# Optimization experiments

Hardware: AMD Instinct MI355X
Metric: run time of the kernel (lower is better)

The kernel has to match this reference:

```python
import jax, jax.numpy as jnp
import numpy as np

N, E, G, D = 50000, 500000, 100, 64
H = D // 64          # num_heads = emb_dim // 64 = 1
HD = D // H          # head_dim


def setup_inputs() -> dict:
    key = jax.random.key(0)
    ks = jax.random.split(key, 14)
    s = 0.05
    return {
        "x": jax.random.normal(ks[0], (N, D), jnp.float32),
        "edge_attr": jax.random.normal(ks[1], (E, D), jnp.float32),
        "u": jax.random.normal(ks[2], (G, D), jnp.float32),
        # params: torch Linear convention, weight is [out, in]
        "W_edge": jax.random.normal(ks[3], (D, 4 * D), jnp.float32) * s,
        "b_edge": jnp.zeros((D,), jnp.float32),
        "W_node": jax.random.normal(ks[4], (D, 4 * D), jnp.float32) * s,
        "b_node": jnp.zeros((D,), jnp.float32),
        "W_glob": jax.random.normal(ks[5], (D, 3 * D), jnp.float32) * s,
        "b_glob": jnp.zeros((D,), jnp.float32),
        # NodeAttn params: w1 Linear(3D->D), w2 [H, HD], w3 Linear(2D->D)
        "na_w1": jax.random.normal(ks[6], (D, 3 * D), jnp.float32) * s,
        "na_b1": jnp.zeros((D,), jnp.float32),
        "na_w2": jax.random.normal(ks[7], (H, HD), jnp.float32) * s,
        "na_w3": jax.random.normal(ks[8], (D, 2 * D), jnp.float32) * s,
        "na_b3": jnp.zeros((D,), jnp.float32),
        "edge_index": jax.random.randint(ks[9], (2, E), 0, N),
        "node_batch": jnp.sort(jax.random.randint(ks[10], (N,), 0, G)),
        "edge_batch": jnp.sort(jax.random.randint(ks[11], (E,), 0, G)),
    }


def reference(x, edge_attr, u, W_edge, b_edge, W_node, b_node, W_glob, b_glob,
              na_w1, na_b1, na_w2, na_w3, na_b3,
              edge_index, node_batch, edge_batch):
    row, col = edge_index[0], edge_index[1]

    # ---- edge model: gather + concat + MLP ----
    e_in = jnp.concatenate([edge_attr, x[row], x[col], u[edge_batch]], axis=1)  # [E, 4D]
    edge_new = jax.nn.relu(e_in @ W_edge.T + b_edge)                             # [E, D]

    # ---- NodeAttn: segment softmax attention, scatter-sum to nodes ----
    def node_attn(q, k_v, k_e, idx):
        h = (jnp.concatenate([q, k_v, k_e], axis=1) @ na_w1.T + na_b1)  # [E, D]
        h = jax.nn.leaky_relu(h.reshape(-1, H, HD))
        w = jnp.einsum('nhc,hc->nh', h, na_w2)[:, :, None]              # [E, H, 1]
        m = jax.ops.segment_max(w, idx, num_segments=N)
        ex = jnp.exp(w - m[idx])
        sm = jax.ops.segment_sum(ex, idx, num_segments=N)
        p = ex / (sm[idx] + 1e-16)                                      # segment softmax
        v = (jnp.concatenate([k_v, k_e], axis=1) @ na_w3.T + na_b3).reshape(-1, H, HD)
        return jax.ops.segment_sum((p * v).reshape(-1, D), idx, num_segments=N)

    sent = node_attn(x[row], x[col], edge_new, row)   # [N, D]
    recv = node_attn(x[col], x[row], edge_new, col)   # [N, D]

    # ---- node model ----
    n_in = jnp.concatenate([x, sent, recv, u[node_batch]], axis=1)  # [N, 4D]
    x_new = jax.nn.relu(n_in @ W_node.T + b_node)                   # [N, D]

    # ---- global model: scatter-aggregate nodes/edges per graph ----
    node_agg = jax.ops.segment_sum(x_new, node_batch, num_segments=G)
    edge_agg = jax.ops.segment_sum(edge_new, edge_batch, num_segments=G)
    g_in = jnp.concatenate([u, node_agg, edge_agg], axis=1)         # [G, 3D]
    u_new = jax.nn.relu(g_in @ W_glob.T + b_glob)                   # [G, D]

    return (x_new, edge_new, u_new)
```

## Files before the change

### kernel.cpp

```cpp
#include <hip/hip_runtime.h>

typedef __attribute__((ext_vector_type(8))) short bf16x8;
typedef __attribute__((ext_vector_type(4))) float f32x4;

#define MFMA16(A, B, C) __builtin_amdgcn_mfma_f32_16x16x32_bf16(A, B, C, 0, 0, 0)

__device__ __forceinline__ float4 ld4(const float* p) {
  return *reinterpret_cast<const float4*>(p);
}

__device__ __forceinline__ unsigned short f2bf(float f) {
  unsigned u = __float_as_uint(f);
  unsigned r = u + 0x7FFFu + ((u >> 16) & 1u);
  return (unsigned short)(r >> 16);
}

__device__ __forceinline__ float bf2f(unsigned short b) {
  return __uint_as_float(((unsigned)b) << 16);
}
__device__ __forceinline__ float bflo(unsigned u) { return __uint_as_float(u << 16); }
__device__ __forceinline__ float bfhi(unsigned u) { return __uint_as_float(u & 0xFFFF0000u); }
__device__ __forceinline__ unsigned bfpack(float lo, float hi) {
  return (unsigned)f2bf(lo) | ((unsigned)f2bf(hi) << 16);
}

__device__ __forceinline__ bf16x8 cvt8(float4 a, float4 b) {
  bf16x8 v;
  v[0] = (short)f2bf(a.x); v[1] = (short)f2bf(a.y);
  v[2] = (short)f2bf(a.z); v[3] = (short)f2bf(a.w);
  v[4] = (short)f2bf(b.x); v[5] = (short)f2bf(b.y);
  v[6] = (short)f2bf(b.z); v[7] = (short)f2bf(b.w);
  return v;
}

__global__ void __launch_bounds__(256) k_fill(
    const int* __restrict__ row, const int* __restrict__ col,
    int* __restrict__ deg_s, int* __restrict__ deg_r,
    int* __restrict__ lst_s, int* __restrict__ lst_r, int E) {
  int e = blockIdx.x * 256 + threadIdx.x;
  if (e >= E) return;
  int r = row[e], c = col[e];
  int s0 = atomicAdd(deg_s + r, 1);
  if (s0 < 64) lst_s[(size_t)r * 64 + s0] = e;
  int s1 = atomicAdd(deg_r + c, 1);
  if (s1 < 64) lst_r[(size_t)c * 64 + s1] = e;
}

__global__ void __launch_bounds__(128) k_precomb(
    const float* __restrict__ Wn, const float* __restrict__ W3, const float* __restrict__ b3,
    const float* __restrict__ We, const float* __restrict__ u_,
    float* __restrict__ Ms, float* __restrict__ cs,
    float* __restrict__ Mr, float* __restrict__ cr,
    float* __restrict__ pu, float* __restrict__ pun, int G) {
  int t = threadIdx.x;
  if (blockIdx.x < 8) {
    int dir = t >> 6, o = t & 63;
    const float* wrow = Wn + (size_t)o * 256 + 64 + 64 * dir;
    float* M  = dir ? Mr : Ms;
    float* cv = dir ? cr : cs;
    if (blockIdx.x == 0) {
      float cb = 0.f;
      for (int k = 0; k < 64; ++k) cb = fmaf(wrow[k], b3[k], cb);
      cv[o] = cb;
    }
    int c0 = blockIdx.x * 16;
    for (int c = c0; c < c0 + 16; ++c) {
      float m = 0.f;
      for (int k = 0; k < 64; ++k) m = fmaf(wrow[k], W3[k * 128 + c], m);
      M[(size_t)o * 128 + c] = m;
    }
  } else {
    const float* W = (blockIdx.x == 8) ? We : Wn;
    float* dst = (blockIdx.x == 8) ? pu : pun;
    int o = t & 63;
    const float* wr = W + (size_t)o * 256 + 192;
    for (int g = t >> 6; g < G; g += 2) {
      float a = 0.f;
      const float* uv = u_ + (size_t)g * 64;
      for (int k = 0; k < 64; ++k) a = fmaf(wr[k], uv[k], a);
      dst[(size_t)g * 64 + o] = a;
    }
  }
}

__global__ void __launch_bounds__(256) k_pack(
    const float* __restrict__ We, const float* __restrict__ W1, const float* __restrict__ Wn,
    const float* __restrict__ Ms, const float* __restrict__ Mr,
    unsigned short* __restrict__ BpP, unsigned short* __restrict__ BpN) {
  int idx = blockIdx.x * 256 + threadIdx.x;
  if (idx < 2048) {
    int lane = idx & 63, nt = (idx >> 6) & 15, ks = idx >> 10;
    int l15 = lane & 15, lg = lane >> 4;
    int c = nt * 16 + l15, a = c >> 6, o = c & 63;
    bf16x8 v;
    #pragma unroll
    for (int j = 0; j < 8; ++j) {
      int k = ks * 32 + lg * 8 + j;
      float f = (a == 0) ? We[o * 256 + 64 + k]
              : (a == 1) ? We[o * 256 + 128 + k]
              : (a == 2) ? W1[o * 192 + k]
                         : W1[o * 192 + 64 + k];
      v[j] = (short)f2bf(f);
    }
    *(bf16x8*)(BpP + (size_t)idx * 8) = v;
  } else if (idx < 2048 + 2560) {
    int i2 = idx - 2048;
    int lane = i2 & 63, nt = (i2 >> 6) & 3, ks = i2 >> 8;
    int l15 = lane & 15, lg = lane >> 4;
    int col = nt * 16 + l15;
    bf16x8 v;
    #pragma unroll
    for (int j = 0; j < 8; ++j) {
      int k = ks * 32 + lg * 8 + j;
      float f = (k < 64) ? Wn[col * 256 + k]
              : (k < 192) ? Ms[col * 128 + (k - 64)]
                          : Mr[col * 128 + (k - 192)];
      v[j] = (short)f2bf(f);
    }
    *(bf16x8*)(BpN + (size_t)i2 * 8) = v;
  }
}

__global__ void __launch_bounds__(256) k_nodepre4(
    const float* __restrict__ x, const unsigned short* __restrict__ BpP,
    unsigned int* __restrict__ pxx, unsigned int* __restrict__ hqk,
    unsigned short* __restrict__ x_bf, int N) {
  __shared__ unsigned short lB[2048 * 8];
  const int tid = threadIdx.x;
  for (int i = tid; i < 2048; i += 256)
    *(uint4*)(lB + (size_t)i * 8) = *(const uint4*)(BpP + (size_t)i * 8);
  __syncthreads();
  const int lane = tid & 63, wid = tid >> 6, l15 = lane & 15, lg = lane >> 4;
  const int n0 = (blockIdx.x * 4 + wid) * 16;
  if (n0 >= N) return;
  int arow = n0 + l15; if (arow >= N) arow = N - 1;
  const float* src = x + (size_t)arow * 64 + lg * 8;
  bf16x8 A0 = cvt8(ld4(src), ld4(src + 4));
  bf16x8 A1 = cvt8(ld4(src + 32), ld4(src + 36));
  if (n0 + l15 < N) {
    *(bf16x8*)(x_bf + (size_t)(n0 + l15) * 64 + lg * 8) = A0;
    *(bf16x8*)(x_bf + (size_t)(n0 + l15) * 64 + 32 + lg * 8) = A1;
  }
  f32x4 acc[16];
  #pragma unroll
  for (int nt = 0; nt < 16; ++nt) {
    acc[nt] = (f32x4){0.f, 0.f, 0.f, 0.f};
    acc[nt] = MFMA16(A0, *(const bf16x8*)(lB + ((size_t)(0 * 16 + nt) * 64 + lane) * 8), acc[nt]);
    acc[nt] = MFMA16(A1, *(const bf16x8*)(lB + ((size_t)(1 * 16 + nt) * 64 + lane) * 8), acc[nt]);
  }
  #pragma unroll
  for (int q = 0; q < 4; ++q) {
    const int o = q * 16 + l15;
    #pragma unroll
    for (int j = 0; j < 4; ++j) {
      int n = n0 + lg * 4 + j;
      if (n < N) {
        pxx[(size_t)n * 64 + o] = bfpack(acc[q][j],     acc[4 + q][j]);
        hqk[(size_t)n * 64 + o] = bfpack(acc[8 + q][j], acc[12 + q][j]);
      }
    }
  }
}

__global__ void __launch_bounds__(256, 2) k_edgeattn4(
    const float* __restrict__ ea,
    const unsigned int* __restrict__ pxx, const unsigned int* __restrict__ hqk,
    const float* __restrict__ pu,
    const float* __restrict__ We, const float* __restrict__ be,
    const float* __restrict__ W1, const float* __restrict__ b1, const float* __restrict__ w2,
    const int* __restrict__ row, const int* __restrict__ col, const int* __restrict__ ebat,
    float* __restrict__ edge_out, unsigned short* __restrict__ en_bf,
    float* __restrict__ w_s, float* __restrict__ w_r, int E) {
  __shared__ unsigned short enl_all[4][16 * 64];
  const int tid = threadIdx.x, lane = tid & 63, wid = tid >> 6;
  const int l15 = lane & 15, lg = lane >> 4;

  bf16x8 B1[4][2], B2[4][2];
  #pragma unroll
  for (int nt = 0; nt < 4; ++nt) {
    #pragma unroll
    for (int ks = 0; ks < 2; ++ks) {
      const float* s1 = We + (size_t)(nt * 16 + l15) * 256 + ks * 32 + lg * 8;
      B1[nt][ks] = cvt8(ld4(s1), ld4(s1 + 4));
      const float* s2 = W1 + (size_t)(nt * 16 + l15) * 192 + 128 + ks * 32 + lg * 8;
      B2[nt][ks] = cvt8(ld4(s2), ld4(s2 + 4));
    }
  }
  float be_l[4], b1_l[4], w2_l[4];
  #pragma unroll
  for (int nt = 0; nt < 4; ++nt) {
    be_l[nt] = be[nt * 16 + l15];
    b1_l[nt] = b1[nt * 16 + l15];
    w2_l[nt] = w2[nt * 16 + l15];
  }
  unsigned short* enl = enl_all[wid];
  const int nwaves = gridDim.x * 4;
  const int swz_r = (l15 & 7) << 4;

  for (int e0 = (blockIdx.x * 4 + wid) * 16; e0 < E; e0 += nwaves * 16) {
    int rj[4], cj[4], gj[4];
    if (e0 + 16 <= E) {
      int4 r4 = *(const int4*)(row + e0 + lg * 4);
      int4 c4 = *(const int4*)(col + e0 + lg * 4);
      int4 g4 = *(const int4*)(ebat + e0 + lg * 4);
      rj[0]=r4.x; rj[1]=r4.y; rj[2]=r4.z; rj[3]=r4.w;
      cj[0]=c4.x; cj[1]=c4.y; cj[2]=c4.z; cj[3]=c4.w;
      gj[0]=g4.x; gj[1]=g4.y; gj[2]=g4.z; gj[3]=g4.w;
    } else {
      #pragma unroll
      for (int j = 0; j < 4; ++j) {
        int ee = e0 + lg * 4 + j; if (ee >= E) ee = E - 1;
        rj[j] = row[ee]; cj[j] = col[ee]; gj[j] = ebat[ee];
      }
    }

    unsigned hr_[4][4], hc_[4][4], pr_[4][4], pc_[4][4];
    float puv[4][4];
    #pragma unroll
    for (int j = 0; j < 4; ++j) {
      #pragma unroll
      for (int nt = 0; nt < 4; ++nt) {
        const int o = nt * 16 + l15;
        hr_[j][nt] = hqk[(size_t)rj[j] * 64 + o];
        hc_[j][nt] = hqk[(size_t)cj[j] * 64 + o];
        pr_[j][nt] = pxx[(size_t)rj[j] * 64 + o];
        pc_[j][nt] = pxx[(size_t)cj[j] * 64 + o];
        puv[j][nt] = pu [(size_t)gj[j] * 64 + o];
      }
    }

    int erow = e0 + l15; if (erow >= E) erow = E - 1;
    const float* arow = ea + (size_t)erow * 64;
    bf16x8 A1[2];
    #pragma unroll
    for (int ks = 0; ks < 2; ++ks) {
      const float* s = arow + ks * 32 + lg * 8;
      A1[ks] = cvt8(ld4(s), ld4(s + 4));
    }

    f32x4 acc[4];
    #pragma unroll
    for (int nt = 0; nt < 4; ++nt) acc[nt] = (f32x4){0.f, 0.f, 0.f, 0.f};
    #pragma unroll
    for (int nt = 0; nt < 4; ++nt) {
      acc[nt] = MFMA16(A1[0], B1[nt][0], acc[nt]);
      acc[nt] = MFMA16(A1[1], B1[nt][1], acc[nt]);
    }

    #pragma unroll
    for (int j = 0; j < 4; ++j) {
      const int m = lg * 4 + j;
      const bool st = (e0 + m) < E;
      float* eo = edge_out + (size_t)(e0 + m) * 64 + l15;
      unsigned short* eb = en_bf + (size_t)(e0 + m) * 64 + l15;
      const int rbase = m * 128, sw = (m & 7) << 4;
      #pragma unroll
      for (int nt = 0; nt < 4; ++nt) {
        float v = acc[nt][j] + be_l[nt] + bflo(pr_[j][nt]) + bfhi(pc_[j][nt]) + puv[j][nt];
        v = fmaxf(v, 0.f);
        unsigned short bv = f2bf(v);
        if (st) { eo[nt * 16] = v; eb[nt * 16] = bv; }
        int byte = rbase + ((nt * 32 + l15 * 2) ^ sw);
        *(unsigned short*)((char*)enl + byte) = bv;
      }
    }

    asm volatile("s_waitcnt lgkmcnt(0)" ::: "memory");
    bf16x8 A2[2];
    #pragma unroll
    for (int ks = 0; ks < 2; ++ks) {
      int byte = l15 * 128 + (((ks * 64) + lg * 16) ^ swz_r);
      A2[ks] = *(const bf16x8*)((const char*)enl + byte);
    }

    f32x4 tac[4];
    #pragma unroll
    for (int nt = 0; nt < 4; ++nt) tac[nt] = (f32x4){0.f, 0.f, 0.f, 0.f};
    #pragma unroll
    for (int nt = 0; nt < 4; ++nt) {
      tac[nt] = MFMA16(A2[0], B2[nt][0], tac[nt]);
      tac[nt] = MFMA16(A2[1], B2[nt][1], tac[nt]);
    }

    float as4[4] = {0.f, 0.f, 0.f, 0.f}, ar4[4] = {0.f, 0.f, 0.f, 0.f};
    #pragma unroll
    for (int j = 0; j < 4; ++j) {
      #pragma unroll
      for (int nt = 0; nt < 4; ++nt) {
        float tt = tac[nt][j] + b1_l[nt];
        float hs = tt + bflo(hr_[j][nt]) + bfhi(hc_[j][nt]); hs = (hs >= 0.f) ? hs : 0.01f * hs;
        float hr2 = tt + bflo(hc_[j][nt]) + bfhi(hr_[j][nt]); hr2 = (hr2 >= 0.f) ? hr2 : 0.01f * hr2;
        as4[j] = fmaf(hs, w2_l[nt], as4[j]);
        ar4[j] = fmaf(hr2, w2_l[nt], ar4[j]);
      }
    }
    #pragma unroll
    for (int j = 0; j < 4; ++j) {
      #pragma unroll
      for (int d = 1; d < 16; d <<= 1) {
        as4[j] += __shfl_xor(as4[j], d, 64);
        ar4[j] += __shfl_xor(ar4[j], d, 64);
      }
    }
    if (l15 == 0) {
      #pragma unroll
      for (int j = 0; j < 4; ++j) {
        int e = e0 + lg * 4 + j;
        if (e < E) { w_s[e] = as4[j]; w_r[e] = ar4[j]; }
      }
    }
  }
}

__global__ void __launch_bounds__(256) k_gatherw2(
    const unsigned short* __restrict__ x_bf, const unsigned short* __restrict__ en_bf,
    const float* __restrict__ w_s, const float* __restrict__ w_r,
    const int* __restrict__ lst_s, const int* __restrict__ lst_r,
    const int* __restrict__ deg_s, const int* __restrict__ deg_r,
    const int* __restrict__ row, const int* __restrict__ col,
    unsigned short* __restrict__ ss_s, unsigned short* __restrict__ ss_r,
    float* __restrict__ gam_s, float* __restrict__ gam_r, int N) {
  const int dir = blockIdx.y;
  const float* w = dir ? w_r : w_s;
  const int* lst = dir ? lst_r : lst_s;
  const int* deg_a = dir ? deg_r : deg_s;
  const int* other_idx = dir ? row : col;
  unsigned short* ss = dir ? ss_r : ss_s;
  float* gam = dir ? gam_r : gam_s;

  int wid = threadIdx.x >> 6, lane = threadIdx.x & 63;
  int n = blockIdx.x * 4 + wid;
  if (n >= N) return;
  int deg = deg_a[n];
  deg = deg < 64 ? deg : 64;
  unsigned short* ssd = ss + (size_t)n * 128;
  if (deg == 0) {
    ssd[lane] = 0; ssd[64 + lane] = 0;
    if (lane == 0) gam[n] = 0.f;
    return;
  }
  int e = 0, oe = 0;
  float wv = -1e30f;
  if (lane < deg) {
    e = lst[(size_t)n * 64 + lane];
    oe = other_idx[e];
    wv = w[e];
  }
  float m = wv;
  #pragma unroll
  for (int d = 32; d; d >>= 1) m = fmaxf(m, __shfl_xor(m, d, 64));
  float p = (lane < deg) ? __expf(wv - m) : 0.f;
  float S = p;
  #pragma unroll
  for (int d = 32; d; d >>= 1) S += __shfl_xor(S, d, 64);
  float sx4[4] = {0.f, 0.f, 0.f, 0.f};
  float se4[4] = {0.f, 0.f, 0.f, 0.f};
  int i = 0;
  for (; i + 8 <= deg; i += 8) {
    float pp[8]; int oo[8], ee[8];
    #pragma unroll
    for (int k = 0; k < 8; ++k) {
      pp[k] = __shfl(p, i + k, 64);
      oo[k] = __shfl(oe, i + k, 64);
      ee[k] = __shfl(e, i + k, 64);
    }
    float xv[8], ev[8];
    #pragma unroll
    for (int k = 0; k < 8; ++k) {
      xv[k] = bf2f(x_bf[(size_t)oo[k] * 64 + lane]);
      ev[k] = bf2f(en_bf[(size_t)ee[k] * 64 + lane]);
    }
    #pragma unroll
    for (int k = 0; k < 8; ++k) {
      sx4[k & 3] = fmaf(pp[k], xv[k], sx4[k & 3]);
      se4[k & 3] = fmaf(pp[k], ev[k], se4[k & 3]);
    }
  }
  for (; i + 4 <= deg; i += 4) {
    float pp[4]; int oo[4], ee[4];
    #pragma unroll
    for (int k = 0; k < 4; ++k) {
      pp[k] = __shfl(p, i + k, 64);
      oo[k] = __shfl(oe, i + k, 64);
      ee[k] = __shfl(e, i + k, 64);
    }
    #pragma unroll
    for (int k = 0; k < 4; ++k) {
      sx4[k] = fmaf(pp[k], bf2f(x_bf[(size_t)oo[k] * 64 + lane]), sx4[k]);
      se4[k] = fmaf(pp[k], bf2f(en_bf[(size_t)ee[k] * 64 + lane]), se4[k]);
    }
  }
  for (; i < deg; ++i) {
    float pi = __shfl(p, i, 64);
    int ei = __shfl(e, i, 64);
    int oi = __shfl(oe, i, 64);
    sx4[0] = fmaf(pi, bf2f(x_bf[(size_t)oi * 64 + lane]), sx4[0]);
    se4[0] = fmaf(pi, bf2f(en_bf[(size_t)ei * 64 + lane]), se4[0]);
  }
  float sx = (sx4[0] + sx4[1]) + (sx4[2] + sx4[3]);
  float se = (se4[0] + se4[1]) + (se4[2] + se4[3]);
  float inv = 1.f / (S + 1e-16f);
  ssd[lane] = f2bf(sx * inv);
  ssd[64 + lane] = f2bf(se * inv);
  if (lane == 0) gam[n] = S * inv;
}

__global__ void __launch_bounds__(256) k_node4(
    const unsigned short* __restrict__ x_bf,
    const unsigned short* __restrict__ ss_s, const unsigned short* __restrict__ ss_r,
    const float* __restrict__ gam_s, const float* __restrict__ gam_r,
    const unsigned short* __restrict__ BpN,
    const float* __restrict__ bn, const float* __restrict__ cs, const float* __restrict__ cr,
    const float* __restrict__ pun, const int* __restrict__ nbat,
    float* __restrict__ x_out, int N) {
  __shared__ unsigned short lB[2560 * 8];
  const int tid = threadIdx.x;
  for (int i = tid; i < 2560; i += 256)
    *(uint4*)(lB + (size_t)i * 8) = *(const uint4*)(BpN + (size_t)i * 8);
  __syncthreads();
  const int lane = tid & 63, wid = tid >> 6, l15 = lane & 15, lg = lane >> 4;
  const int n0 = (blockIdx.x * 4 + wid) * 16;
  if (n0 >= N) return;
  int arow = n0 + l15; if (arow >= N) arow = N - 1;

  f32x4 acc[4];
  #pragma unroll
  for (int nt = 0; nt < 4; ++nt) acc[nt] = (f32x4){0.f, 0.f, 0.f, 0.f};

  #pragma unroll
  for (int ks = 0; ks < 10; ++ks) {
    const unsigned short* s;
    if (ks < 2)      s = x_bf + (size_t)arow * 64  + ks * 32 + lg * 8;
    else if (ks < 6) s = ss_s + (size_t)arow * 128 + (ks - 2) * 32 + lg * 8;
    else             s = ss_r + (size_t)arow * 128 + (ks - 6) * 32 + lg * 8;
    bf16x8 A = *(const bf16x8*)s;
    #pragma unroll
    for (int nt = 0; nt < 4; ++nt)
      acc[nt] = MFMA16(A, *(const bf16x8*)(lB + ((size_t)(ks * 4 + nt) * 64 + lane) * 8), acc[nt]);
  }

  #pragma unroll
  for (int j = 0; j < 4; ++j) {
    int n = n0 + lg * 4 + j;
    int nn = n < N ? n : N - 1;
    int g = nbat[nn];
    float gs = gam_s[nn], gr = gam_r[nn];
    #pragma unroll
    for (int nt = 0; nt < 4; ++nt) {
      int o = nt * 16 + l15;
      float v = acc[nt][j] + bn[o] + pun[(size_t)g * 64 + o] + gs * cs[o] + gr * cr[o];
      v = fmaxf(v, 0.f);
      if (n < N) x_out[(size_t)n * 64 + o] = v;
    }
  }
}

__global__ void __launch_bounds__(256) k_segsum(
    const float* __restrict__ vals, const int* __restrict__ seg,
    float* __restrict__ out, int n) {
  int d = threadIdx.x & 63;
  int grp = threadIdx.x >> 6;
  long base = (long)blockIdx.x * 256 + (long)grp * 64;
  float sum = 0.f;
  int cur = -1;
  for (int k = 0; k < 64; ++k) {
    long e = base + k;
    if (e >= n) break;
    int gb = seg[e];
    float v = vals[e * 64 + d];
    if (gb != cur) {
      if (cur >= 0) atomicAdd(out + (size_t)cur * 64 + d, sum);
      cur = gb; sum = v;
    } else {
      sum += v;
    }
  }
  if (cur >= 0) atomicAdd(out + (size_t)cur * 64 + d, sum);
}

__global__ void __launch_bounds__(256) k_segsum_bf(
    const unsigned short* __restrict__ vals, const int* __restrict__ seg,
    float* __restrict__ out, int n) {
  int d = threadIdx.x & 63;
  int grp = threadIdx.x >> 6;
  long base = (long)blockIdx.x * 256 + (long)grp * 64;
  float sum = 0.f;
  int cur = -1;
  for (int k = 0; k < 64; ++k) {
    long e = base + k;
    if (e >= n) break;
    int gb = seg[e];
    float v = bf2f(vals[e * 64 + d]);
    if (gb != cur) {
      if (cur >= 0) atomicAdd(out + (size_t)cur * 64 + d, sum);
      cur = gb; sum = v;
    } else {
      sum += v;
    }
  }
  if (cur >= 0) atomicAdd(out + (size_t)cur * 64 + d, sum);
}

__global__ void __launch_bounds__(64) k_glob(
    const float* __restrict__ u, const float* __restrict__ nagg, const float* __restrict__ eagg,
    const float* __restrict__ Wg, const float* __restrict__ bg,
    float* __restrict__ u_out, int G) {
  int t = blockIdx.x * 64 + threadIdx.x;
  if (t >= G * 64) return;
  int g = t >> 6, o = t & 63;
  float acc = bg[o];
  const float* wr = Wg + (size_t)o * 192;
  for (int i = 0; i < 64; ++i) acc = fmaf(u[g * 64 + i],    wr[i],       acc);
  for (int i = 0; i < 64; ++i) acc = fmaf(nagg[g * 64 + i], wr[64 + i],  acc);
  for (int i = 0; i < 64; ++i) acc = fmaf(eagg[g * 64 + i], wr[128 + i], acc);
  u_out[t] = fmaxf(acc, 0.f);
}

extern "C" void kernel_launch(void* const* d_in, const int* in_sizes, int n_in,
                              void* d_out, int out_size, void* d_ws, size_t ws_size,
                              hipStream_t stream) {
  const float* x   = (const float*)d_in[0];
  const float* ea  = (const float*)d_in[1];
  const float* u   = (const float*)d_in[2];
  const float* We  = (const float*)d_in[3];
  const float* be  = (const float*)d_in[4];
  const float* Wn  = (const float*)d_in[5];
  const float* bn  = (const float*)d_in[6];
  const float* Wg  = (const float*)d_in[7];
  const float* bg  = (const float*)d_in[8];
  const float* W1  = (const float*)d_in[9];
  const float* b1  = (const float*)d_in[10];
  const float* w2  = (const float*)d_in[11];
  const float* W3  = (const float*)d_in[12];
  const float* b3  = (const float*)d_in[13];
  const int* eidx  = (const int*)d_in[14];
  const int* nbat  = (const int*)d_in[15];
  const int* ebat  = (const int*)d_in[16];

  const int N = in_sizes[0] / 64;
  const int E = in_sizes[1] / 64;
  const int G = in_sizes[2] / 64;
  const int* row = eidx;
  const int* col = eidx + E;

  float* out   = (float*)d_out;
  float* x_out = out;
  float* e_out = out + (size_t)N * 64;
  float* u_out = out + (size_t)(N + E) * 64;

  float* ws = (float*)d_ws;
  unsigned int* pxx = (unsigned int*)ws;
  unsigned int* hqk = pxx + (size_t)N * 64;
  unsigned short* ss_s = (unsigned short*)pxx;
  unsigned short* ss_r = (unsigned short*)hqk;
  unsigned short* x_bf = (unsigned short*)(hqk + (size_t)N * 64);
  float* w_s = (float*)(x_bf + (size_t)N * 64);
  float* w_r = w_s + E;
  float* pu  = w_r + E;
  float* pun = pu + (size_t)G * 64;
  int* lst_s = (int*)(pun + (size_t)G * 64);
  int* lst_r = lst_s + (size_t)N * 64;
  int* deg_s = lst_r + (size_t)N * 64;
  int* deg_r = deg_s + N;
  float* nagg = (float*)(deg_r + N);
  float* eagg = nagg + (size_t)G * 64;
  float* gam_s = eagg + (size_t)G * 64;
  float* gam_r = gam_s + N;
  float* Ms = gam_r + N;
  float* Mr = Ms + 64 * 128;
  float* cs = Mr + 64 * 128;
  float* cr = cs + 64;
  unsigned short* BpP = (unsigned short*)(cr + 64);
  unsigned short* BpN = BpP + 2048 * 8;
  unsigned short* en_bf = BpN + 2560 * 8;

  hipMemsetAsync(deg_s, 0, (2 * (size_t)N + 2 * (size_t)G * 64) * sizeof(int), stream);

  const int gE = (E + 255) / 256;
  const int gT = (N / 16 + 3) / 4;

  k_fill<<<gE, 256, 0, stream>>>(row, col, deg_s, deg_r, lst_s, lst_r, E);
  k_precomb<<<10, 128, 0, stream>>>(Wn, W3, b3, We, u, Ms, cs, Mr, cr, pu, pun, G);
  k_pack<<<18, 256, 0, stream>>>(We, W1, Wn, Ms, Mr, BpP, BpN);
  k_nodepre4<<<gT, 256, 0, stream>>>(x, BpP, pxx, hqk, x_bf, N);
  k_edgeattn4<<<2048, 256, 0, stream>>>(ea, pxx, hqk, pu, We, be, W1, b1, w2,
                                        row, col, ebat, e_out, en_bf, w_s, w_r, E);
  k_segsum_bf<<<(E + 255) / 256, 256, 0, stream>>>(en_bf, ebat, eagg, E);
  k_gatherw2<<<dim3((N + 3) / 4, 2), 256, 0, stream>>>(
      x_bf, en_bf, w_s, w_r, lst_s, lst_r, deg_s, deg_r, row, col,
      ss_s, ss_r, gam_s, gam_r, N);
  k_node4<<<gT, 256, 0, stream>>>(x_bf, ss_s, ss_r, gam_s, gam_r, BpN, bn, cs, cr,
                                  pun, nbat, x_out, N);
  k_segsum<<<(N + 255) / 256, 256, 0, stream>>>(x_out, nbat, nagg, N);
  k_glob<<<(G * 64 + 63) / 64, 64, 0, stream>>>(u, nagg, eagg, Wg, bg, u_out, G);
}
```

Measured before the change: 456.6 us.

## Interleave node projections, prefetch edge indices, and merge both gather directions

Node pre-projection now writes pxx and hqk interleaved as one uint2 per element, so the edge kernel gathers both values for a node with a single 8-byte load instead of two 4-byte loads. The edge-attention loop loads next iteration's row/col/batch indices early, a software prefetch that shortens the dependent-load chain. The gather kernel handles the sent and received directions in one wave per node instead of two blocks via blockIdx.y, overlapping their loads but looping to the larger degree. The cost is more live registers and some wasted iterations when the two degrees differ.

```diff
diff --git a/kernel.cpp b/kernel.cpp
--- a/kernel.cpp
+++ b/kernel.cpp
@@ -121,10 +121,9 @@
   }
 }
 
-__global__ void __launch_bounds__(256) k_nodepre4(
+__global__ void __launch_bounds__(256) k_nodepre5(
     const float* __restrict__ x, const unsigned short* __restrict__ BpP,
-    unsigned int* __restrict__ pxx, unsigned int* __restrict__ hqk,
-    unsigned short* __restrict__ x_bf, int N) {
+    uint2* __restrict__ phq, unsigned short* __restrict__ x_bf, int N) {
   __shared__ unsigned short lB[2048 * 8];
   const int tid = threadIdx.x;
   for (int i = tid; i < 2048; i += 256)
@@ -155,17 +154,18 @@
     for (int j = 0; j < 4; ++j) {
       int n = n0 + lg * 4 + j;
       if (n < N) {
-        pxx[(size_t)n * 64 + o] = bfpack(acc[q][j],     acc[4 + q][j]);
-        hqk[(size_t)n * 64 + o] = bfpack(acc[8 + q][j], acc[12 + q][j]);
-      }
-    }
-  }
-}
-
-__global__ void __launch_bounds__(256, 2) k_edgeattn4(
+        uint2 v;
+        v.x = bfpack(acc[q][j],     acc[4 + q][j]);
+        v.y = bfpack(acc[8 + q][j], acc[12 + q][j]);
+        phq[(size_t)n * 64 + o] = v;
+      }
+    }
+  }
+}
+
+__global__ void __launch_bounds__(256, 2) k_edgeattn5(
     const float* __restrict__ ea,
-    const unsigned int* __restrict__ pxx, const unsigned int* __restrict__ hqk,
-    const float* __restrict__ pu,
+    const uint2* __restrict__ phq, const float* __restrict__ pu,
     const float* __restrict__ We, const float* __restrict__ be,
     const float* __restrict__ W1, const float* __restrict__ b1, const float* __restrict__ w2,
     const int* __restrict__ row, const int* __restrict__ col, const int* __restrict__ ebat,
@@ -195,37 +195,39 @@
   }
   unsigned short* enl = enl_all[wid];
   const int nwaves = gridDim.x * 4;
+  const int step = nwaves * 16;
   const int swz_r = (l15 & 7) << 4;
-
-  for (int e0 = (blockIdx.x * 4 + wid) * 16; e0 < E; e0 += nwaves * 16) {
-    int rj[4], cj[4], gj[4];
-    if (e0 + 16 <= E) {
-      int4 r4 = *(const int4*)(row + e0 + lg * 4);
-      int4 c4 = *(const int4*)(col + e0 + lg * 4);
-      int4 g4 = *(const int4*)(ebat + e0 + lg * 4);
+  const int start = (blockIdx.x * 4 + wid) * 16;
+
+  int rj[4], cj[4], gj[4];
+  if (start < E) {
+    if (start + 16 <= E) {
+      int4 r4 = *(const int4*)(row + start + lg * 4);
+      int4 c4 = *(const int4*)(col + start + lg * 4);
+      int4 g4 = *(const int4*)(ebat + start + lg * 4);
       rj[0]=r4.x; rj[1]=r4.y; rj[2]=r4.z; rj[3]=r4.w;
       cj[0]=c4.x; cj[1]=c4.y; cj[2]=c4.z; cj[3]=c4.w;
       gj[0]=g4.x; gj[1]=g4.y; gj[2]=g4.z; gj[3]=g4.w;
     } else {
       #pragma unroll
       for (int j = 0; j < 4; ++j) {
-        int ee = e0 + lg * 4 + j; if (ee >= E) ee = E - 1;
+        int ee = start + lg * 4 + j; if (ee >= E) ee = E - 1;
         rj[j] = row[ee]; cj[j] = col[ee]; gj[j] = ebat[ee];
       }
     }
-
-    unsigned hr_[4][4], hc_[4][4], pr_[4][4], pc_[4][4];
+  }
+
+  for (int e0 = start; e0 < E; e0 += step) {
+    uint2 vr[4][4], vc[4][4];
     float puv[4][4];
     #pragma unroll
     for (int j = 0; j < 4; ++j) {
       #pragma unroll
       for (int nt = 0; nt < 4; ++nt) {
         const int o = nt * 16 + l15;
-        hr_[j][nt] = hqk[(size_t)rj[j] * 64 + o];
-        hc_[j][nt] = hqk[(size_t)cj[j] * 64 + o];
-        pr_[j][nt] = pxx[(size_t)rj[j] * 64 + o];
-        pc_[j][nt] = pxx[(size_t)cj[j] * 64 + o];
-        puv[j][nt] = pu [(size_t)gj[j] * 64 + o];
+        vr[j][nt] = phq[(size_t)rj[j] * 64 + o];
+        vc[j][nt] = phq[(size_t)cj[j] * 64 + o];
+        puv[j][nt] = pu[(size_t)gj[j] * 64 + o];
       }
     }
 
@@ -236,6 +238,25 @@
     for (int ks = 0; ks < 2; ++ks) {
       const float* s = arow + ks * 32 + lg * 8;
       A1[ks] = cvt8(ld4(s), ld4(s + 4));
+    }
+
+    int rn[4] = {0,0,0,0}, cn[4] = {0,0,0,0}, gn[4] = {0,0,0,0};
+    const int e1 = e0 + step;
+    if (e1 < E) {
+      if (e1 + 16 <= E) {
+        int4 r4 = *(const int4*)(row + e1 + lg * 4);
+        int4 c4 = *(const int4*)(col + e1 + lg * 4);
+        int4 g4 = *(const int4*)(ebat + e1 + lg * 4);
+        rn[0]=r4.x; rn[1]=r4.y; rn[2]=r4.z; rn[3]=r4.w;
+        cn[0]=c4.x; cn[1]=c4.y; cn[2]=c4.z; cn[3]=c4.w;
+        gn[0]=g4.x; gn[1]=g4.y; gn[2]=g4.z; gn[3]=g4.w;
+      } else {
+        #pragma unroll
+        for (int j = 0; j < 4; ++j) {
+          int ee = e1 + lg * 4 + j; if (ee >= E) ee = E - 1;
+          rn[j] = row[ee]; cn[j] = col[ee]; gn[j] = ebat[ee];
+        }
+      }
     }
 
     f32x4 acc[4];
@@ -256,7 +277,7 @@
       const int rbase = m * 128, sw = (m & 7) << 4;
       #pragma unroll
       for (int nt = 0; nt < 4; ++nt) {
-        float v = acc[nt][j] + be_l[nt] + bflo(pr_[j][nt]) + bfhi(pc_[j][nt]) + puv[j][nt];
+        float v = acc[nt][j] + be_l[nt] + bflo(vr[j][nt].x) + bfhi(vc[j][nt].x) + puv[j][nt];
         v = fmaxf(v, 0.f);
         unsigned short bv = f2bf(v);
         if (st) { eo[nt * 16] = v; eb[nt * 16] = bv; }
@@ -288,8 +309,8 @@
       #pragma unroll
       for (int nt = 0; nt < 4; ++nt) {
         float tt = tac[nt][j] + b1_l[nt];
-        float hs = tt + bflo(hr_[j][nt]) + bfhi(hc_[j][nt]); hs = (hs >= 0.f) ? hs : 0.01f * hs;
-        float hr2 = tt + bflo(hc_[j][nt]) + bfhi(hr_[j][nt]); hr2 = (hr2 >= 0.f) ? hr2 : 0.01f * hr2;
+        float hs = tt + bflo(vr[j][nt].y) + bfhi(vc[j][nt].y); hs = (hs >= 0.f) ? hs : 0.01f * hs;
+        float hr2 = tt + bflo(vc[j][nt].y) + bfhi(vr[j][nt].y); hr2 = (hr2 >= 0.f) ? hr2 : 0.01f * hr2;
         as4[j] = fmaf(hs, w2_l[nt], as4[j]);
         ar4[j] = fmaf(hr2, w2_l[nt], ar4[j]);
       }
@@ -309,100 +330,87 @@
         if (e < E) { w_s[e] = as4[j]; w_r[e] = ar4[j]; }
       }
     }
-  }
-}
-
-__global__ void __launch_bounds__(256) k_gatherw2(
+
+    #pragma unroll
+    for (int j = 0; j < 4; ++j) { rj[j] = rn[j]; cj[j] = cn[j]; gj[j] = gn[j]; }
+  }
+}
+
+__global__ void __launch_bounds__(256) k_gatherw3(
     const unsigned short* __restrict__ x_bf, const unsigned short* __restrict__ en_bf,
     const float* __restrict__ w_s, const float* __restrict__ w_r,
     const int* __restrict__ lst_s, const int* __restrict__ lst_r,
-    const int* __restrict__ deg_s, const int* __restrict__ deg_r,
+    const int* __restrict__ deg_sa, const int* __restrict__ deg_ra,
     const int* __restrict__ row, const int* __restrict__ col,
     unsigned short* __restrict__ ss_s, unsigned short* __restrict__ ss_r,
     float* __restrict__ gam_s, float* __restrict__ gam_r, int N) {
-  const int dir = blockIdx.y;
-  const float* w = dir ? w_r : w_s;
-  const int* lst = dir ? lst_r : lst_s;
-  const int* deg_a = dir ? deg_r : deg_s;
-  const int* other_idx = dir ? row : col;
-  unsigned short* ss = dir ? ss_r : ss_s;
-  float* gam = dir ? gam_r : gam_s;
-
   int wid = threadIdx.x >> 6, lane = threadIdx.x & 63;
   int n = blockIdx.x * 4 + wid;
   if (n >= N) return;
-  int deg = deg_a[n];
-  deg = deg < 64 ? deg : 64;
-  unsigned short* ssd = ss + (size_t)n * 128;
-  if (deg == 0) {
-    ssd[lane] = 0; ssd[64 + lane] = 0;
-    if (lane == 0) gam[n] = 0.f;
-    return;
-  }
-  int e = 0, oe = 0;
-  float wv = -1e30f;
-  if (lane < deg) {
-    e = lst[(size_t)n * 64 + lane];
-    oe = other_idx[e];
-    wv = w[e];
-  }
-  float m = wv;
-  #pragma unroll
-  for (int d = 32; d; d >>= 1) m = fmaxf(m, __shfl_xor(m, d, 64));
-  float p = (lane < deg) ? __expf(wv - m) : 0.f;
-  float S = p;
-  #pragma unroll
-  for (int d = 32; d; d >>= 1) S += __shfl_xor(S, d, 64);
-  float sx4[4] = {0.f, 0.f, 0.f, 0.f};
-  float se4[4] = {0.f, 0.f, 0.f, 0.f};
-  int i = 0;
-  for (; i + 8 <= deg; i += 8) {
-    float pp[8]; int oo[8], ee[8];
-    #pragma unroll
-    for (int k = 0; k < 8; ++k) {
-      pp[k] = __shfl(p, i + k, 64);
-      oo[k] = __shfl(oe, i + k, 64);
-      ee[k] = __shfl(e, i + k, 64);
-    }
-    float xv[8], ev[8];
-    #pragma unroll
-    for (int k = 0; k < 8; ++k) {
-      xv[k] = bf2f(x_bf[(size_t)oo[k] * 64 + lane]);
-      ev[k] = bf2f(en_bf[(size_t)ee[k] * 64 + lane]);
-    }
-    #pragma unroll
-    for (int k = 0; k < 8; ++k) {
-      sx4[k & 3] = fmaf(pp[k], xv[k], sx4[k & 3]);
-      se4[k & 3] = fmaf(pp[k], ev[k], se4[k & 3]);
-    }
-  }
-  for (; i + 4 <= deg; i += 4) {
-    float pp[4]; int oo[4], ee[4];
+  int ds = deg_sa[n]; ds = ds < 64 ? ds : 64;
+  int dr = deg_ra[n]; dr = dr < 64 ? dr : 64;
+  unsigned short* ssd_s = ss_s + (size_t)n * 128;
+  unsigned short* ssd_r = ss_r + (size_t)n * 128;
+
+  int es = 0, oes = 0, er = 0, oer = 0;
+  float wvs = -1e30f, wvr = -1e30f;
+  if (lane < ds) { es = lst_s[(size_t)n * 64 + lane]; oes = col[es]; wvs = w_s[es]; }
+  if (lane < dr) { er = lst_r[(size_t)n * 64 + lane]; oer = row[er]; wvr = w_r[er]; }
+  float ms = wvs, mr = wvr;
+  #pragma unroll
+  for (int d = 32; d; d >>= 1) {
+    ms = fmaxf(ms, __shfl_xor(ms, d, 64));
+    mr = fmaxf(mr, __shfl_xor(mr, d, 64));
+  }
+  float ps = (lane < ds) ? __expf(wvs - ms) : 0.f;
+  float pr = (lane < dr) ? __expf(wvr - mr) : 0.f;
+  float Ss = ps, Sr = pr;
+  #pragma unroll
+  for (int d = 32; d; d >>= 1) {
+    Ss += __shfl_xor(Ss, d, 64);
+    Sr += __shfl_xor(Sr, d, 64);
+  }
+  float sxs[2] = {0.f, 0.f}, ses[2] = {0.f, 0.f};
+  float sxr[2] = {0.f, 0.f}, ser[2] = {0.f, 0.f};
+  int dm = ds > dr ? ds : dr;
+  for (int i = 0; i < dm; i += 4) {
+    float pps[4], ppr[4];
+    int oos[4], ees[4], oor[4], eer[4];
     #pragma unroll
     for (int k = 0; k < 4; ++k) {
-      pp[k] = __shfl(p, i + k, 64);
-      oo[k] = __shfl(oe, i + k, 64);
-      ee[k] = __shfl(e, i + k, 64);
-    }
+      pps[k] = __shfl(ps, i + k, 64);
+      ppr[k] = __shfl(pr, i + k, 64);
+      oos[k] = __shfl(oes, i + k, 64);
+      ees[k] = __shfl(es, i + k, 64);
+      oor[k] = __shfl(oer, i + k, 64);
+      eer[k] = __shfl(er, i + k, 64);
+    }
+    float xvs[4], evs[4], xvr[4], evr[4];
     #pragma unroll
     for (int k = 0; k < 4; ++k) {
-      sx4[k] = fmaf(pp[k], bf2f(x_bf[(size_t)oo[k] * 64 + lane]), sx4[k]);
-      se4[k] = fmaf(pp[k], bf2f(en_bf[(size_t)ee[k] * 64 + lane]), se4[k]);
-    }
-  }
-  for (; i < deg; ++i) {
-    float pi = __shfl(p, i, 64);
-    int ei = __shfl(e, i, 64);
-    int oi = __shfl(oe, i, 64);
-    sx4[0] = fmaf(pi, bf2f(x_bf[(size_t)oi * 64 + lane]), sx4[0]);
-    se4[0] = fmaf(pi, bf2f(en_bf[(size_t)ei * 64 + lane]), se4[0]);
-  }
-  float sx = (sx4[0] + sx4[1]) + (sx4[2] + sx4[3]);
-  float se = (se4[0] + se4[1]) + (se4[2] + se4[3]);
-  float inv = 1.f / (S + 1e-16f);
-  ssd[lane] = f2bf(sx * inv);
-  ssd[64 + lane] = f2bf(se * inv);
-  if (lane == 0) gam[n] = S * inv;
+      xvs[k] = bf2f(x_bf[(size_t)oos[k] * 64 + lane]);
+      evs[k] = bf2f(en_bf[(size_t)ees[k] * 64 + lane]);
+      xvr[k] = bf2f(x_bf[(size_t)oor[k] * 64 + lane]);
+      evr[k] = bf2f(en_bf[(size_t)eer[k] * 64 + lane]);
+    }
+    #pragma unroll
+    for (int k = 0; k < 4; ++k) {
+      sxs[k & 1] = fmaf(pps[k], xvs[k], sxs[k & 1]);
+      ses[k & 1] = fmaf(pps[k], evs[k], ses[k & 1]);
+      sxr[k & 1] = fmaf(ppr[k], xvr[k], sxr[k & 1]);
+      ser[k & 1] = fmaf(ppr[k], evr[k], ser[k & 1]);
+    }
+  }
+  float invs = 1.f / (Ss + 1e-16f);
+  float invr = 1.f / (Sr + 1e-16f);
+  ssd_s[lane]      = f2bf((sxs[0] + sxs[1]) * invs);
+  ssd_s[64 + lane] = f2bf((ses[0] + ses[1]) * invs);
+  ssd_r[lane]      = f2bf((sxr[0] + sxr[1]) * invr);
+  ssd_r[64 + lane] = f2bf((ser[0] + ser[1]) * invr);
+  if (lane == 0) {
+    gam_s[n] = (ds > 0) ? Ss * invs : 0.f;
+    gam_r[n] = (dr > 0) ? Sr * invr : 0.f;
+  }
 }
 
 __global__ void __launch_bounds__(256) k_node4(
@@ -549,11 +557,10 @@
   float* u_out = out + (size_t)(N + E) * 64;
 
   float* ws = (float*)d_ws;
-  unsigned int* pxx = (unsigned int*)ws;
-  unsigned int* hqk = pxx + (size_t)N * 64;
-  unsigned short* ss_s = (unsigned short*)pxx;
-  unsigned short* ss_r = (unsigned short*)hqk;
-  unsigned short* x_bf = (unsigned short*)(hqk + (size_t)N * 64);
+  uint2* phq = (uint2*)ws;
+  unsigned short* ss_s = (unsigned short*)ws;
+  unsigned short* ss_r = (unsigned short*)(ws + (size_t)N * 64);
+  unsigned short* x_bf = (unsigned short*)(ws + (size_t)N * 128);
   float* w_s = (float*)(x_bf + (size_t)N * 64);
   float* w_r = w_s + E;
   float* pu  = w_r + E;
@@ -582,11 +589,11 @@
   k_fill<<<gE, 256, 0, stream>>>(row, col, deg_s, deg_r, lst_s, lst_r, E);
   k_precomb<<<10, 128, 0, stream>>>(Wn, W3, b3, We, u, Ms, cs, Mr, cr, pu, pun, G);
   k_pack<<<18, 256, 0, stream>>>(We, W1, Wn, Ms, Mr, BpP, BpN);
-  k_nodepre4<<<gT, 256, 0, stream>>>(x, BpP, pxx, hqk, x_bf, N);
-  k_edgeattn4<<<2048, 256, 0, stream>>>(ea, pxx, hqk, pu, We, be, W1, b1, w2,
+  k_nodepre5<<<gT, 256, 0, stream>>>(x, BpP, phq, x_bf, N);
+  k_edgeattn5<<<2048, 256, 0, stream>>>(ea, phq, pu, We, be, W1, b1, w2,
                                         row, col, ebat, e_out, en_bf, w_s, w_r, E);
   k_segsum_bf<<<(E + 255) / 256, 256, 0, stream>>>(en_bf, ebat, eagg, E);
-  k_gatherw2<<<dim3((N + 3) / 4, 2), 256, 0, stream>>>(
+  k_gatherw3<<<(N + 3) / 4, 256, 0, stream>>>(
       x_bf, en_bf, w_s, w_r, lst_s, lst_r, deg_s, deg_r, row, col,
       ss_s, ss_r, gam_s, gam_r, N);
   k_node4<<<gT, 256, 0, stream>>>(x_bf, ss_s, ss_r, gam_s, gam_r, BpN, bn, cs, cr,
```

New measurement: 467.6 us. 1.02x slower.

## Interleave node projections, stage edge weights in LDS, prefetch next edge indices

Applied to the files above, without the earlier changes.

Node precompute now writes the pxx and hqk projections interleaved as one uint2 per element, so each gathered edge endpoint needs one 8-byte load instead of two 4-byte loads from separate arrays. The edge-attention kernel moves its bf16 B-operand weights from registers into shared memory and prefetches the next iteration's row/col/batch indices. This frees registers, so launch bounds rise to 5 waves per SIMD and the grid drops to 1280 blocks. The costs are extra LDS reads per MFMA and more LDS per block.

```diff
diff --git a/kernel.cpp b/kernel.cpp
--- a/kernel.cpp
+++ b/kernel.cpp
@@ -121,10 +121,9 @@
   }
 }
 
-__global__ void __launch_bounds__(256) k_nodepre4(
+__global__ void __launch_bounds__(256) k_nodepre5(
     const float* __restrict__ x, const unsigned short* __restrict__ BpP,
-    unsigned int* __restrict__ pxx, unsigned int* __restrict__ hqk,
-    unsigned short* __restrict__ x_bf, int N) {
+    uint2* __restrict__ phq, unsigned short* __restrict__ x_bf, int N) {
   __shared__ unsigned short lB[2048 * 8];
   const int tid = threadIdx.x;
   for (int i = tid; i < 2048; i += 256)
@@ -155,37 +154,39 @@
     for (int j = 0; j < 4; ++j) {
       int n = n0 + lg * 4 + j;
       if (n < N) {
-        pxx[(size_t)n * 64 + o] = bfpack(acc[q][j],     acc[4 + q][j]);
-        hqk[(size_t)n * 64 + o] = bfpack(acc[8 + q][j], acc[12 + q][j]);
-      }
-    }
-  }
-}
-
-__global__ void __launch_bounds__(256, 2) k_edgeattn4(
+        uint2 v;
+        v.x = bfpack(acc[q][j],     acc[4 + q][j]);
+        v.y = bfpack(acc[8 + q][j], acc[12 + q][j]);
+        phq[(size_t)n * 64 + o] = v;
+      }
+    }
+  }
+}
+
+__global__ void __launch_bounds__(256, 5) k_edgeattn6(
     const float* __restrict__ ea,
-    const unsigned int* __restrict__ pxx, const unsigned int* __restrict__ hqk,
-    const float* __restrict__ pu,
+    const uint2* __restrict__ phq, const float* __restrict__ pu,
     const float* __restrict__ We, const float* __restrict__ be,
     const float* __restrict__ W1, const float* __restrict__ b1, const float* __restrict__ w2,
     const int* __restrict__ row, const int* __restrict__ col, const int* __restrict__ ebat,
     float* __restrict__ edge_out, unsigned short* __restrict__ en_bf,
     float* __restrict__ w_s, float* __restrict__ w_r, int E) {
+  __shared__ unsigned short B1l[512 * 8];
+  __shared__ unsigned short B2l[512 * 8];
   __shared__ unsigned short enl_all[4][16 * 64];
   const int tid = threadIdx.x, lane = tid & 63, wid = tid >> 6;
   const int l15 = lane & 15, lg = lane >> 4;
 
-  bf16x8 B1[4][2], B2[4][2];
-  #pragma unroll
-  for (int nt = 0; nt < 4; ++nt) {
-    #pragma unroll
-    for (int ks = 0; ks < 2; ++ks) {
-      const float* s1 = We + (size_t)(nt * 16 + l15) * 256 + ks * 32 + lg * 8;
-      B1[nt][ks] = cvt8(ld4(s1), ld4(s1 + 4));
-      const float* s2 = W1 + (size_t)(nt * 16 + l15) * 192 + 128 + ks * 32 + lg * 8;
-      B2[nt][ks] = cvt8(ld4(s2), ld4(s2 + 4));
-    }
-  }
+  for (int i = tid; i < 512; i += 256) {
+    int li = i & 63, nt = (i >> 6) & 3, ks = i >> 8;
+    int l15i = li & 15, lgi = li >> 4;
+    const float* s1 = We + (size_t)(nt * 16 + l15i) * 256 + ks * 32 + lgi * 8;
+    *(bf16x8*)(B1l + (size_t)i * 8) = cvt8(ld4(s1), ld4(s1 + 4));
+    const float* s2 = W1 + (size_t)(nt * 16 + l15i) * 192 + 128 + ks * 32 + lgi * 8;
+    *(bf16x8*)(B2l + (size_t)i * 8) = cvt8(ld4(s2), ld4(s2 + 4));
+  }
+  __syncthreads();
+
   float be_l[4], b1_l[4], w2_l[4];
   #pragma unroll
   for (int nt = 0; nt < 4; ++nt) {
@@ -195,37 +196,39 @@
   }
   unsigned short* enl = enl_all[wid];
   const int nwaves = gridDim.x * 4;
+  const int step = nwaves * 16;
   const int swz_r = (l15 & 7) << 4;
-
-  for (int e0 = (blockIdx.x * 4 + wid) * 16; e0 < E; e0 += nwaves * 16) {
-    int rj[4], cj[4], gj[4];
-    if (e0 + 16 <= E) {
-      int4 r4 = *(const int4*)(row + e0 + lg * 4);
-      int4 c4 = *(const int4*)(col + e0 + lg * 4);
-      int4 g4 = *(const int4*)(ebat + e0 + lg * 4);
+  const int start = (blockIdx.x * 4 + wid) * 16;
+
+  int rj[4], cj[4], gj[4];
+  if (start < E) {
+    if (start + 16 <= E) {
+      int4 r4 = *(const int4*)(row + start + lg * 4);
+      int4 c4 = *(const int4*)(col + start + lg * 4);
+      int4 g4 = *(const int4*)(ebat + start + lg * 4);
       rj[0]=r4.x; rj[1]=r4.y; rj[2]=r4.z; rj[3]=r4.w;
       cj[0]=c4.x; cj[1]=c4.y; cj[2]=c4.z; cj[3]=c4.w;
       gj[0]=g4.x; gj[1]=g4.y; gj[2]=g4.z; gj[3]=g4.w;
     } else {
       #pragma unroll
       for (int j = 0; j < 4; ++j) {
-        int ee = e0 + lg * 4 + j; if (ee >= E) ee = E - 1;
+        int ee = start + lg * 4 + j; if (ee >= E) ee = E - 1;
         rj[j] = row[ee]; cj[j] = col[ee]; gj[j] = ebat[ee];
       }
     }
-
-    unsigned hr_[4][4], hc_[4][4], pr_[4][4], pc_[4][4];
+  }
+
+  for (int e0 = start; e0 < E; e0 += step) {
+    uint2 vr[4][4], vc[4][4];
     float puv[4][4];
     #pragma unroll
     for (int j = 0; j < 4; ++j) {
       #pragma unroll
       for (int nt = 0; nt < 4; ++nt) {
         const int o = nt * 16 + l15;
-        hr_[j][nt] = hqk[(size_t)rj[j] * 64 + o];
-        hc_[j][nt] = hqk[(size_t)cj[j] * 64 + o];
-        pr_[j][nt] = pxx[(size_t)rj[j] * 64 + o];
-        pc_[j][nt] = pxx[(size_t)cj[j] * 64 + o];
-        puv[j][nt] = pu [(size_t)gj[j] * 64 + o];
+        vr[j][nt] = phq[(size_t)rj[j] * 64 + o];
+        vc[j][nt] = phq[(size_t)cj[j] * 64 + o];
+        puv[j][nt] = pu[(size_t)gj[j] * 64 + o];
       }
     }
 
@@ -238,13 +241,35 @@
       A1[ks] = cvt8(ld4(s), ld4(s + 4));
     }
 
+    int rn[4] = {0,0,0,0}, cn[4] = {0,0,0,0}, gn[4] = {0,0,0,0};
+    const int e1 = e0 + step;
+    if (e1 < E) {
+      if (e1 + 16 <= E) {
+        int4 r4 = *(const int4*)(row + e1 + lg * 4);
+        int4 c4 = *(const int4*)(col + e1 + lg * 4);
+        int4 g4 = *(const int4*)(ebat + e1 + lg * 4);
+        rn[0]=r4.x; rn[1]=r4.y; rn[2]=r4.z; rn[3]=r4.w;
+        cn[0]=c4.x; cn[1]=c4.y; cn[2]=c4.z; cn[3]=c4.w;
+        gn[0]=g4.x; gn[1]=g4.y; gn[2]=g4.z; gn[3]=g4.w;
+      } else {
+        #pragma unroll
+        for (int j = 0; j < 4; ++j) {
+          int ee = e1 + lg * 4 + j; if (ee >= E) ee = E - 1;
+          rn[j] = row[ee]; cn[j] = col[ee]; gn[j] = ebat[ee];
+        }
+      }
+    }
+
     f32x4 acc[4];
     #pragma unroll
     for (int nt = 0; nt < 4; ++nt) acc[nt] = (f32x4){0.f, 0.f, 0.f, 0.f};
     #pragma unroll
-    for (int nt = 0; nt < 4; ++nt) {
-      acc[nt] = MFMA16(A1[0], B1[nt][0], acc[nt]);
-      acc[nt] = MFMA16(A1[1], B1[nt][1], acc[nt]);
+    for (int ks = 0; ks < 2; ++ks) {
+      #pragma unroll
+      for (int nt = 0; nt < 4; ++nt) {
+        bf16x8 B = *(const bf16x8*)(B1l + ((size_t)(ks * 256 + nt * 64 + lane)) * 8);
+        acc[nt] = MFMA16(A1[ks], B, acc[nt]);
+      }
     }
 
     #pragma unroll
@@ -256,7 +281,7 @@
       const int rbase = m * 128, sw = (m & 7) << 4;
       #pragma unroll
       for (int nt = 0; nt < 4; ++nt) {
-        float v = acc[nt][j] + be_l[nt] + bflo(pr_[j][nt]) + bfhi(pc_[j][nt]) + puv[j][nt];
+        float v = acc[nt][j] + be_l[nt] + bflo(vr[j][nt].x) + bfhi(vc[j][nt].x) + puv[j][nt];
         v = fmaxf(v, 0.f);
         unsigned short bv = f2bf(v);
         if (st) { eo[nt * 16] = v; eb[nt * 16] = bv; }
@@ -277,9 +302,12 @@
     #pragma unroll
     for (int nt = 0; nt < 4; ++nt) tac[nt] = (f32x4){0.f, 0.f, 0.f, 0.f};
     #pragma unroll
-    for (int nt = 0; nt < 4; ++nt) {
-      tac[nt] = MFMA16(A2[0], B2[nt][0], tac[nt]);
-      tac[nt] = MFMA16(A2[1], B2[nt][1], tac[nt]);
+    for (int ks = 0; ks < 2; ++ks) {
+      #pragma unroll
+      for (int nt = 0; nt < 4; ++nt) {
+        bf16x8 B = *(const bf16x8*)(B2l + ((size_t)(ks * 256 + nt * 64 + lane)) * 8);
+        tac[nt] = MFMA16(A2[ks], B, tac[nt]);
+      }
     }
 
     float as4[4] = {0.f, 0.f, 0.f, 0.f}, ar4[4] = {0.f, 0.f, 0.f, 0.f};
@@ -288,8 +316,8 @@
       #pragma unroll
       for (int nt = 0; nt < 4; ++nt) {
         float tt = tac[nt][j] + b1_l[nt];
-        float hs = tt + bflo(hr_[j][nt]) + bfhi(hc_[j][nt]); hs = (hs >= 0.f) ? hs : 0.01f * hs;
-        float hr2 = tt + bflo(hc_[j][nt]) + bfhi(hr_[j][nt]); hr2 = (hr2 >= 0.f) ? hr2 : 0.01f * hr2;
+        float hs = tt + bflo(vr[j][nt].y) + bfhi(vc[j][nt].y); hs = (hs >= 0.f) ? hs : 0.01f * hs;
+        float hr2 = tt + bflo(vc[j][nt].y) + bfhi(vr[j][nt].y); hr2 = (hr2 >= 0.f) ? hr2 : 0.01f * hr2;
         as4[j] = fmaf(hs, w2_l[nt], as4[j]);
         ar4[j] = fmaf(hr2, w2_l[nt], ar4[j]);
       }
@@ -309,6 +337,9 @@
         if (e < E) { w_s[e] = as4[j]; w_r[e] = ar4[j]; }
       }
     }
+
+    #pragma unroll
+    for (int j = 0; j < 4; ++j) { rj[j] = rn[j]; cj[j] = cn[j]; gj[j] = gn[j]; }
   }
 }
 
@@ -549,11 +580,10 @@
   float* u_out = out + (size_t)(N + E) * 64;
 
   float* ws = (float*)d_ws;
-  unsigned int* pxx = (unsigned int*)ws;
-  unsigned int* hqk = pxx + (size_t)N * 64;
-  unsigned short* ss_s = (unsigned short*)pxx;
-  unsigned short* ss_r = (unsigned short*)hqk;
-  unsigned short* x_bf = (unsigned short*)(hqk + (size_t)N * 64);
+  uint2* phq = (uint2*)ws;
+  unsigned short* ss_s = (unsigned short*)ws;
+  unsigned short* ss_r = (unsigned short*)(ws + (size_t)N * 64);
+  unsigned short* x_bf = (unsigned short*)(ws + (size_t)N * 128);
   float* w_s = (float*)(x_bf + (size_t)N * 64);
   float* w_r = w_s + E;
   float* pu  = w_r + E;
@@ -582,8 +612,8 @@
   k_fill<<<gE, 256, 0, stream>>>(row, col, deg_s, deg_r, lst_s, lst_r, E);
   k_precomb<<<10, 128, 0, stream>>>(Wn, W3, b3, We, u, Ms, cs, Mr, cr, pu, pun, G);
   k_pack<<<18, 256, 0, stream>>>(We, W1, Wn, Ms, Mr, BpP, BpN);
-  k_nodepre4<<<gT, 256, 0, stream>>>(x, BpP, pxx, hqk, x_bf, N);
-  k_edgeattn4<<<2048, 256, 0, stream>>>(ea, pxx, hqk, pu, We, be, W1, b1, w2,
+  k_nodepre5<<<gT, 256, 0, stream>>>(x, BpP, phq, x_bf, N);
+  k_edgeattn6<<<1280, 256, 0, stream>>>(ea, phq, pu, We, be, W1, b1, w2,
                                         row, col, ebat, e_out, en_bf, w_s, w_r, E);
   k_segsum_bf<<<(E + 255) / 256, 256, 0, stream>>>(en_bf, ebat, eagg, E);
   k_gatherw2<<<dim3((N + 3) / 4, 2), 256, 0, stream>>>(
```

After: 706.4 us. 1.55x slower.
